# Performance work log

Hardware: AMD Instinct MI355X
Metric: run time of the kernel (lower is better)

## Reference

```python
import jax, jax.numpy as jnp
import numpy as np

B, D = 32768, 512
L, K = 4, 1024


def setup_inputs() -> dict:
    key = jax.random.key(0)
    kz, kc = jax.random.split(key)
    z = jax.random.normal(kz, (B, D), dtype=jnp.float32)
    # nn.Parameter(torch.randn(L, K, D) * 0.1)
    codebooks = jax.random.normal(kc, (L, K, D), dtype=jnp.float32) * 0.1
    return {"z": z, "codebooks": codebooks}


def reference(z, codebooks):
    # z: [B, D], codebooks: [L, K, D]
    num_levels = codebooks.shape[0]
    residual = z
    level_vecs = []
    rq_loss = jnp.float32(0.0)
    for l in range(num_levels):  # small fixed L, structurally distinct levels
        cb = codebooks[l]  # [K, D]
        # squared euclidean distance via ||r||^2 - 2 r.c + ||c||^2 (same math as
        # sum((r[:,None]-c[None])**2, -1), avoids the [B,K,D] broadcast intermediate)
        r2 = jnp.sum(residual * residual, axis=-1, keepdims=True)      # [B, 1]
        c2 = jnp.sum(cb * cb, axis=-1)                                  # [K]
        dist = r2 - 2.0 * (residual @ cb.T) + c2                        # [B, K]
        idx = jnp.argmin(dist, axis=-1)                                 # [B]
        chosen = cb[idx]                                                # [B, D]
        level_vecs.append(chosen)
        residual = residual - chosen
        # F.mse_loss(residual.detach(), zeros) -> mean of squared residual, no grad
        rq_loss = rq_loss + jnp.mean(jax.lax.stop_gradient(residual) ** 2)
    all_level_vectors = jnp.stack(level_vecs, axis=0)  # [L, B, D]
    quantized = all_level_vectors.sum(axis=0)          # [B, D]
    return (quantized, all_level_vectors, rq_loss)
```

## Files before the change

### kernel.cpp

```cpp
#include <hip/hip_runtime.h>

#define BROWS 32768
#define DIM   512
#define NK    1024
#define NL    4

typedef _Float16 f16;
typedef _Float16 f16x8 __attribute__((ext_vector_type(8)));
typedef float f32x4 __attribute__((ext_vector_type(4)));

union H4 { f16 h[4]; ushort4 u; };

__device__ __forceinline__ void split2(float x, f16& h, f16& l) {
  h = (f16)x;
  l = (f16)((x - (float)h) * 4096.0f);
}

__device__ __forceinline__ void gload16(const void* g, const void* l) {
  __builtin_amdgcn_global_load_lds(
      (const __attribute__((address_space(1))) void*)g,
      (__attribute__((address_space(3))) void*)l, 16, 0, 0);
}

__global__ __launch_bounds__(64) void k_pre(const float* __restrict__ cb,
                                            float* __restrict__ c2all,
                                            float* __restrict__ loss_slot,
                                            f16* __restrict__ cbh,
                                            f16* __restrict__ cbl) {
  const int code = blockIdx.x;
  const int lane = threadIdx.x;
  const float4* c4 = (const float4*)(cb + (size_t)code * DIM);
  float s = 0.f;
#pragma unroll
  for (int j = 0; j < 2; ++j) {
    const int e = lane + j * 64;
    const float4 v = c4[e];
    s += v.x * v.x + v.y * v.y + v.z * v.z + v.w * v.w;
    H4 hh, ll;
#pragma unroll
    for (int c = 0; c < 4; ++c) split2((&v.x)[c], hh.h[c], ll.h[c]);
    *(ushort4*)(cbh + (size_t)code * DIM + e * 4) = hh.u;
    *(ushort4*)(cbl + (size_t)code * DIM + e * 4) = ll.u;
  }
#pragma unroll
  for (int m = 1; m < 64; m <<= 1) s += __shfl_xor(s, m, 64);
  if (lane == 0) c2all[code] = s;
  if (code == 0 && lane == 0) *loss_slot = 0.f;
}

__global__ __launch_bounds__(256) void k_splitz(const float* __restrict__ Z,
                                                float* __restrict__ r2,
                                                f16* __restrict__ Rh,
                                                f16* __restrict__ Rl) {
  const int t = threadIdx.x;
  const int row = blockIdx.x * 8 + (t >> 5);
  const int lane = t & 31;
  const float4* z4 = (const float4*)(Z + (size_t)row * DIM);
  float s = 0.f;
#pragma unroll
  for (int j = 0; j < 4; ++j) {
    const int e = lane + j * 32;
    const float4 v = z4[e];
    s += v.x * v.x + v.y * v.y + v.z * v.z + v.w * v.w;
    H4 hh, ll;
#pragma unroll
    for (int c = 0; c < 4; ++c) split2((&v.x)[c], hh.h[c], ll.h[c]);
    *(ushort4*)(Rh + (size_t)row * DIM + e * 4) = hh.u;
    *(ushort4*)(Rl + (size_t)row * DIM + e * 4) = ll.u;
  }
#pragma unroll
  for (int m = 1; m < 32; m <<= 1) s += __shfl_xor(s, m, 64);
  if (lane == 0) r2[row] = s;
}

__global__ __launch_bounds__(256, 2) void k_gemm(
    const f16* __restrict__ Ah, const f16* __restrict__ Al,
    const f16* __restrict__ Bh, const f16* __restrict__ Bl,
    const float* __restrict__ r2v, const float* __restrict__ c2v,
    float* __restrict__ pmin, int* __restrict__ pidx) {
  __shared__ __align__(16) char smem[2][32768];

  const int t = threadIdx.x;
  const int lane = t & 63, wid = t >> 6;
  const int wr = wid >> 1, wc = wid & 1;
  const int nb = blockIdx.x, mb = blockIdx.y;
  const int rowBase = mb * 128, colBase = nb * 128;
  const int l15 = lane & 15, kg = lane >> 4;

  const char* gA[4]; const char* gB[4];
  int ldsA[4], ldsB[4];
#pragma unroll
  for (int i = 0; i < 4; ++i) {
    const int g = i * 256 + wid * 64 + lane;
    const int r = g >> 3;
    const int u = (g & 7) ^ (r & 7);
    gA[i] = (const char*)((u < 4) ? Ah : Al) + (size_t)(rowBase + r) * 1024 + (u & 3) * 16;
    gB[i] = (const char*)((u < 4) ? Bh : Bl) + (size_t)(colBase + r) * 1024 + (u & 3) * 16;
    ldsA[i] = i * 4096 + wid * 1024;
    ldsB[i] = 16384 + i * 4096 + wid * 1024;
  }

  const f32x4 zero = {0.f, 0.f, 0.f, 0.f};
  f32x4 accH[4][4], accL[4][4];
#pragma unroll
  for (int i = 0; i < 4; ++i)
#pragma unroll
    for (int j = 0; j < 4; ++j) { accH[i][j] = zero; accL[i][j] = zero; }

  auto stage = [&](int buf, int kt) {
    char* s = &smem[buf][0];
#pragma unroll
    for (int i = 0; i < 4; ++i) {
      gload16(gA[i] + kt * 64, s + ldsA[i]);
      gload16(gB[i] + kt * 64, s + ldsB[i]);
    }
  };

  auto compute = [&](int buf) {
    const char* sA = &smem[buf][0];
    const char* sB = sA + 16384;
    f16x8 bhv[4], blv[4];
#pragma unroll
    for (int ni = 0; ni < 4; ++ni) {
      const int c = wc * 64 + ni * 16 + l15;
      const int x = c & 7;
      bhv[ni] = *(const f16x8*)(sB + c * 128 + ((kg ^ x) << 4));
      blv[ni] = *(const f16x8*)(sB + c * 128 + (((4 + kg) ^ x) << 4));
    }
#pragma unroll
    for (int mi = 0; mi < 4; ++mi) {
      const int r = wr * 64 + mi * 16 + l15;
      const int x = r & 7;
      const f16x8 ahv = *(const f16x8*)(sA + r * 128 + ((kg ^ x) << 4));
      const f16x8 alw = *(const f16x8*)(sA + r * 128 + (((4 + kg) ^ x) << 4));
#pragma unroll
      for (int ni = 0; ni < 4; ++ni) {
        accH[mi][ni] = __builtin_amdgcn_mfma_f32_16x16x32_f16(ahv, bhv[ni], accH[mi][ni], 0, 0, 0);
        accL[mi][ni] = __builtin_amdgcn_mfma_f32_16x16x32_f16(ahv, blv[ni], accL[mi][ni], 0, 0, 0);
        accL[mi][ni] = __builtin_amdgcn_mfma_f32_16x16x32_f16(alw, bhv[ni], accL[mi][ni], 0, 0, 0);
      }
    }
  };

  stage(0, 0);
  for (int kt = 0; kt < 16; ++kt) {
    __syncthreads();
    if (kt < 15) stage((kt + 1) & 1, kt + 1);
    compute(kt & 1);
  }

  float* redm = (float*)&smem[0][0];
  int* redi = (int*)(&smem[0][0] + 1024);
  float c2c[4];
#pragma unroll
  for (int ni = 0; ni < 4; ++ni) c2c[ni] = c2v[colBase + wc * 64 + ni * 16 + l15];
#pragma unroll
  for (int mi = 0; mi < 4; ++mi) {
#pragma unroll
    for (int j = 0; j < 4; ++j) {
      const int rloc = wr * 64 + mi * 16 + kg * 4 + j;
      const float r2r = r2v[rowBase + rloc];
      float bm = 3.4e38f; int bi = 0x7fffffff;
#pragma unroll
      for (int ni = 0; ni < 4; ++ni) {
        const int col = colBase + wc * 64 + ni * 16 + l15;
        const float dot = accH[mi][ni][j] + accL[mi][ni][j] * 2.44140625e-4f;
        const float dist = (r2r - 2.0f * dot) + c2c[ni];
        if (dist < bm || (dist == bm && col < bi)) { bm = dist; bi = col; }
      }
#pragma unroll
      for (int m = 1; m < 16; m <<= 1) {
        const float om = __shfl_xor(bm, m, 64);
        const int oi = __shfl_xor(bi, m, 64);
        if (om < bm || (om == bm && oi < bi)) { bm = om; bi = oi; }
      }
      if (l15 == 0) { redm[rloc * 2 + wc] = bm; redi[rloc * 2 + wc] = bi; }
    }
  }
  __syncthreads();
  if (t < 128) {
    float bm = redm[t * 2]; int bi = redi[t * 2];
    const float m1 = redm[t * 2 + 1]; const int i1 = redi[t * 2 + 1];
    if (m1 < bm || (m1 == bm && i1 < bi)) { bm = m1; bi = i1; }
    pmin[(size_t)nb * BROWS + rowBase + t] = bm;
    pidx[(size_t)nb * BROWS + rowBase + t] = bi;
  }
}

__global__ __launch_bounds__(256) void k_update(const float* __restrict__ Rin,
                                                const float* __restrict__ CB,
                                                const float* __restrict__ pminv,
                                                const int* __restrict__ pidxv,
                                                float* __restrict__ chosen_out,
                                                float* __restrict__ Rout,
                                                float* __restrict__ r2out,
                                                float* __restrict__ loss,
                                                const float* __restrict__ Z,
                                                float* __restrict__ Q,
                                                f16* __restrict__ Rh,
                                                f16* __restrict__ Rl,
                                                int last) {
  __shared__ float ls[8];
  const int t = threadIdx.x;
  const int rrow = t >> 5, lane = t & 31;
  const int row = blockIdx.x * 8 + rrow;

  float bm = 3.4e38f;
  int bi = 0x7fffffff;
#pragma unroll
  for (int nbk = 0; nbk < 8; ++nbk) {
    const float m = pminv[(size_t)nbk * BROWS + row];
    const int i = pidxv[(size_t)nbk * BROWS + row];
    if (m < bm || (m == bm && i < bi)) { bm = m; bi = i; }
  }

  const float4* r4 = (const float4*)(Rin + (size_t)row * DIM);
  const float4* c4 = (const float4*)(CB + (size_t)bi * DIM);
  float4* ch4 = (float4*)(chosen_out + (size_t)row * DIM);
  float s = 0.f;
#pragma unroll
  for (int j = 0; j < 4; ++j) {
    const int e = lane + j * 32;
    const float4 r = r4[e];
    const float4 c = c4[e];
    float4 rn;
    rn.x = r.x - c.x; rn.y = r.y - c.y; rn.z = r.z - c.z; rn.w = r.w - c.w;
    ch4[e] = c;
    if (!last) {
      ((float4*)(Rout + (size_t)row * DIM))[e] = rn;
      H4 hh, ll;
#pragma unroll
      for (int cc = 0; cc < 4; ++cc) split2((&rn.x)[cc], hh.h[cc], ll.h[cc]);
      *(ushort4*)(Rh + (size_t)row * DIM + e * 4) = hh.u;
      *(ushort4*)(Rl + (size_t)row * DIM + e * 4) = ll.u;
    } else {
      const float4 zv = ((const float4*)(Z + (size_t)row * DIM))[e];
      float4 qq;
      qq.x = zv.x - rn.x; qq.y = zv.y - rn.y; qq.z = zv.z - rn.z; qq.w = zv.w - rn.w;
      ((float4*)(Q + (size_t)row * DIM))[e] = qq;
    }
    s += rn.x * rn.x + rn.y * rn.y + rn.z * rn.z + rn.w * rn.w;
  }
#pragma unroll
  for (int m = 1; m < 32; m <<= 1) s += __shfl_xor(s, m, 64);
  if (lane == 0) {
    if (!last) r2out[row] = s;
    ls[rrow] = s;
  }
  __syncthreads();
  if (t == 0) {
    float tot = 0.f;
#pragma unroll
    for (int i = 0; i < 8; ++i) tot += ls[i];
    atomicAdd(loss, tot * (1.0f / 16777216.0f));
  }
}

extern "C" void kernel_launch(void* const* d_in, const int* in_sizes, int n_in,
                              void* d_out, int out_size, void* d_ws, size_t ws_size,
                              hipStream_t stream) {
  const float* z  = (const float*)d_in[0];
  const float* cb = (const float*)d_in[1];

  float* q    = (float*)d_out;
  float* alv  = (float*)d_out + (size_t)BROWS * DIM;
  float* loss = (float*)d_out + (size_t)BROWS * DIM * (NL + 1);

  float* c2all = (float*)d_ws;
  float* r2ws  = c2all + NL * NK;
  float* pmin  = r2ws + BROWS;
  int*   pidx  = (int*)(pmin + 8 * BROWS);
  f16*   cbh   = (f16*)(pidx + 8 * BROWS);
  f16*   cbl   = cbh + (size_t)NL * NK * DIM;

  f16* Rh = (f16*)q;
  f16* Rl = Rh + (size_t)BROWS * DIM;

  k_pre<<<NL * NK, 64, 0, stream>>>(cb, c2all, loss, cbh, cbl);
  k_splitz<<<BROWS / 8, 256, 0, stream>>>(z, r2ws, Rh, Rl);

  for (int l = 0; l < NL; ++l) {
    const float* R    = (l == 0) ? z : (alv + (size_t)l * BROWS * DIM);
    const float* cbf  = cb + (size_t)l * NK * DIM;
    k_gemm<<<dim3(8, 256), 256, 0, stream>>>(Rh, Rl,
                                             cbh + (size_t)l * NK * DIM,
                                             cbl + (size_t)l * NK * DIM,
                                             r2ws, c2all + l * NK, pmin, pidx);
    const int last = (l == NL - 1);
    float* chosen = alv + (size_t)l * BROWS * DIM;
    float* Rout   = last ? nullptr : (alv + (size_t)(l + 1) * BROWS * DIM);
    k_update<<<BROWS / 8, 256, 0, stream>>>(R, cbf, pmin, pidx, chosen, Rout,
                                            r2ws, loss, z, q, Rh, Rl, last);
  }
}
```

Before: 1.128 ms.

## Interleave hi/lo fp16 residual rows, drop fp32 residual, remap blocks per XCD

Stores the fp16 high and low halves of each residual and codebook row side by side in one buffer. The update kernel rebuilds the fp32 residual from those halves and overwrites them in place, so it no longer writes or reads a separate fp32 residual array each level. The GEMM grid is remapped so consecutive blocks on the same XCD share row tiles, which is meant to improve L2 reuse. The trade-off is that the residual now carries split-fp16 precision (about 22 bits) from level to level, so error can accumulate across levels.

```diff
diff --git a/kernel.cpp b/kernel.cpp
--- a/kernel.cpp
+++ b/kernel.cpp
@@ -9,6 +9,8 @@
 typedef _Float16 f16x8 __attribute__((ext_vector_type(8)));
 typedef float f32x4 __attribute__((ext_vector_type(4)));
 
+#define LSC 2.44140625e-4f
+
 union H4 { f16 h[4]; ushort4 u; };
 
 __device__ __forceinline__ void split2(float x, f16& h, f16& l) {
@@ -25,11 +27,11 @@
 __global__ __launch_bounds__(64) void k_pre(const float* __restrict__ cb,
                                             float* __restrict__ c2all,
                                             float* __restrict__ loss_slot,
-                                            f16* __restrict__ cbh,
-                                            f16* __restrict__ cbl) {
+                                            f16* __restrict__ cbI) {
   const int code = blockIdx.x;
   const int lane = threadIdx.x;
   const float4* c4 = (const float4*)(cb + (size_t)code * DIM);
+  f16* rowL = cbI + (size_t)code * 1024;
   float s = 0.f;
 #pragma unroll
   for (int j = 0; j < 2; ++j) {
@@ -39,8 +41,8 @@
     H4 hh, ll;
 #pragma unroll
     for (int c = 0; c < 4; ++c) split2((&v.x)[c], hh.h[c], ll.h[c]);
-    *(ushort4*)(cbh + (size_t)code * DIM + e * 4) = hh.u;
-    *(ushort4*)(cbl + (size_t)code * DIM + e * 4) = ll.u;
+    *(ushort4*)(rowL + e * 4) = hh.u;
+    *(ushort4*)(rowL + 512 + e * 4) = ll.u;
   }
 #pragma unroll
   for (int m = 1; m < 64; m <<= 1) s += __shfl_xor(s, m, 64);
@@ -50,12 +52,12 @@
 
 __global__ __launch_bounds__(256) void k_splitz(const float* __restrict__ Z,
                                                 float* __restrict__ r2,
-                                                f16* __restrict__ Rh,
-                                                f16* __restrict__ Rl) {
+                                                f16* __restrict__ RL) {
   const int t = threadIdx.x;
   const int row = blockIdx.x * 8 + (t >> 5);
   const int lane = t & 31;
   const float4* z4 = (const float4*)(Z + (size_t)row * DIM);
+  f16* rowL = RL + (size_t)row * 1024;
   float s = 0.f;
 #pragma unroll
   for (int j = 0; j < 4; ++j) {
@@ -65,8 +67,8 @@
     H4 hh, ll;
 #pragma unroll
     for (int c = 0; c < 4; ++c) split2((&v.x)[c], hh.h[c], ll.h[c]);
-    *(ushort4*)(Rh + (size_t)row * DIM + e * 4) = hh.u;
-    *(ushort4*)(Rl + (size_t)row * DIM + e * 4) = ll.u;
+    *(ushort4*)(rowL + e * 4) = hh.u;
+    *(ushort4*)(rowL + 512 + e * 4) = ll.u;
   }
 #pragma unroll
   for (int m = 1; m < 32; m <<= 1) s += __shfl_xor(s, m, 64);
@@ -74,8 +76,8 @@
 }
 
 __global__ __launch_bounds__(256, 2) void k_gemm(
-    const f16* __restrict__ Ah, const f16* __restrict__ Al,
-    const f16* __restrict__ Bh, const f16* __restrict__ Bl,
+    const f16* __restrict__ A,
+    const f16* __restrict__ Bc,
     const float* __restrict__ r2v, const float* __restrict__ c2v,
     float* __restrict__ pmin, int* __restrict__ pidx) {
   __shared__ __align__(16) char smem[2][32768];
@@ -83,7 +85,10 @@
   const int t = threadIdx.x;
   const int lane = t & 63, wid = t >> 6;
   const int wr = wid >> 1, wc = wid & 1;
-  const int nb = blockIdx.x, mb = blockIdx.y;
+  const int lin = blockIdx.y * 8 + blockIdx.x;
+  const int xcd = lin & 7, kk8 = lin >> 3;
+  const int mb = xcd * 32 + (kk8 >> 3);
+  const int nb = kk8 & 7;
   const int rowBase = mb * 128, colBase = nb * 128;
   const int l15 = lane & 15, kg = lane >> 4;
 
@@ -94,8 +99,9 @@
     const int g = i * 256 + wid * 64 + lane;
     const int r = g >> 3;
     const int u = (g & 7) ^ (r & 7);
-    gA[i] = (const char*)((u < 4) ? Ah : Al) + (size_t)(rowBase + r) * 1024 + (u & 3) * 16;
-    gB[i] = (const char*)((u < 4) ? Bh : Bl) + (size_t)(colBase + r) * 1024 + (u & 3) * 16;
+    const size_t off = (size_t)r * 2048 + (size_t)(u >> 2) * 1024 + (u & 3) * 16;
+    gA[i] = (const char*)A + (size_t)rowBase * 2048 + off;
+    gB[i] = (const char*)Bc + (size_t)colBase * 2048 + off;
     ldsA[i] = i * 4096 + wid * 1024;
     ldsB[i] = 16384 + i * 4096 + wid * 1024;
   }
@@ -164,7 +170,7 @@
 #pragma unroll
       for (int ni = 0; ni < 4; ++ni) {
         const int col = colBase + wc * 64 + ni * 16 + l15;
-        const float dot = accH[mi][ni][j] + accL[mi][ni][j] * 2.44140625e-4f;
+        const float dot = accH[mi][ni][j] + accL[mi][ni][j] * LSC;
         const float dist = (r2r - 2.0f * dot) + c2c[ni];
         if (dist < bm || (dist == bm && col < bi)) { bm = dist; bi = col; }
       }
@@ -187,18 +193,15 @@
   }
 }
 
-__global__ __launch_bounds__(256) void k_update(const float* __restrict__ Rin,
+__global__ __launch_bounds__(256) void k_update(f16* RL,
                                                 const float* __restrict__ CB,
                                                 const float* __restrict__ pminv,
                                                 const int* __restrict__ pidxv,
                                                 float* __restrict__ chosen_out,
-                                                float* __restrict__ Rout,
                                                 float* __restrict__ r2out,
                                                 float* __restrict__ loss,
                                                 const float* __restrict__ Z,
-                                                float* __restrict__ Q,
-                                                f16* __restrict__ Rh,
-                                                f16* __restrict__ Rl,
+                                                float* Q,
                                                 int last) {
   __shared__ float ls[8];
   const int t = threadIdx.x;
@@ -214,25 +217,36 @@
     if (m < bm || (m == bm && i < bi)) { bm = m; bi = i; }
   }
 
-  const float4* r4 = (const float4*)(Rin + (size_t)row * DIM);
+  f16* rowL = RL + (size_t)row * 1024;
+  ushort4 hu[4], lu[4];
+#pragma unroll
+  for (int j = 0; j < 4; ++j) {
+    const int e = lane + j * 32;
+    hu[j] = *(const ushort4*)(rowL + e * 4);
+    lu[j] = *(const ushort4*)(rowL + 512 + e * 4);
+  }
+
   const float4* c4 = (const float4*)(CB + (size_t)bi * DIM);
   float4* ch4 = (float4*)(chosen_out + (size_t)row * DIM);
   float s = 0.f;
 #pragma unroll
   for (int j = 0; j < 4; ++j) {
     const int e = lane + j * 32;
-    const float4 r = r4[e];
     const float4 c = c4[e];
+    H4 hh, llv;
+    hh.u = hu[j]; llv.u = lu[j];
     float4 rn;
-    rn.x = r.x - c.x; rn.y = r.y - c.y; rn.z = r.z - c.z; rn.w = r.w - c.w;
+    rn.x = ((float)hh.h[0] + (float)llv.h[0] * LSC) - c.x;
+    rn.y = ((float)hh.h[1] + (float)llv.h[1] * LSC) - c.y;
+    rn.z = ((float)hh.h[2] + (float)llv.h[2] * LSC) - c.z;
+    rn.w = ((float)hh.h[3] + (float)llv.h[3] * LSC) - c.w;
     ch4[e] = c;
     if (!last) {
-      ((float4*)(Rout + (size_t)row * DIM))[e] = rn;
-      H4 hh, ll;
-#pragma unroll
-      for (int cc = 0; cc < 4; ++cc) split2((&rn.x)[cc], hh.h[cc], ll.h[cc]);
-      *(ushort4*)(Rh + (size_t)row * DIM + e * 4) = hh.u;
-      *(ushort4*)(Rl + (size_t)row * DIM + e * 4) = ll.u;
+      H4 nh, nl;
+#pragma unroll
+      for (int cc = 0; cc < 4; ++cc) split2((&rn.x)[cc], nh.h[cc], nl.h[cc]);
+      *(ushort4*)(rowL + e * 4) = nh.u;
+      *(ushort4*)(rowL + 512 + e * 4) = nl.u;
     } else {
       const float4 zv = ((const float4*)(Z + (size_t)row * DIM))[e];
       float4 qq;
@@ -270,26 +284,20 @@
   float* r2ws  = c2all + NL * NK;
   float* pmin  = r2ws + BROWS;
   int*   pidx  = (int*)(pmin + 8 * BROWS);
-  f16*   cbh   = (f16*)(pidx + 8 * BROWS);
-  f16*   cbl   = cbh + (size_t)NL * NK * DIM;
-
-  f16* Rh = (f16*)q;
-  f16* Rl = Rh + (size_t)BROWS * DIM;
-
-  k_pre<<<NL * NK, 64, 0, stream>>>(cb, c2all, loss, cbh, cbl);
-  k_splitz<<<BROWS / 8, 256, 0, stream>>>(z, r2ws, Rh, Rl);
+  f16*   cbI   = (f16*)(pidx + 8 * BROWS);
+
+  f16* RL = (f16*)q;
+
+  k_pre<<<NL * NK, 64, 0, stream>>>(cb, c2all, loss, cbI);
+  k_splitz<<<BROWS / 8, 256, 0, stream>>>(z, r2ws, RL);
 
   for (int l = 0; l < NL; ++l) {
-    const float* R    = (l == 0) ? z : (alv + (size_t)l * BROWS * DIM);
-    const float* cbf  = cb + (size_t)l * NK * DIM;
-    k_gemm<<<dim3(8, 256), 256, 0, stream>>>(Rh, Rl,
-                                             cbh + (size_t)l * NK * DIM,
-                                             cbl + (size_t)l * NK * DIM,
+    k_gemm<<<dim3(8, 256), 256, 0, stream>>>(RL, cbI + (size_t)l * NK * 1024,
                                              r2ws, c2all + l * NK, pmin, pidx);
     const int last = (l == NL - 1);
-    float* chosen = alv + (size_t)l * BROWS * DIM;
-    float* Rout   = last ? nullptr : (alv + (size_t)(l + 1) * BROWS * DIM);
-    k_update<<<BROWS / 8, 256, 0, stream>>>(R, cbf, pmin, pidx, chosen, Rout,
-                                            r2ws, loss, z, q, Rh, Rl, last);
-  }
-}
+    k_update<<<BROWS / 8, 256, 0, stream>>>(RL, cb + (size_t)l * NK * DIM,
+                                            pmin, pidx,
+                                            alv + (size_t)l * BROWS * DIM,
+                                            r2ws, loss, z, q, last);
+  }
+}
```

Measured after the change: 1.087 ms. 3.7% less time.
